# Optimization experiments

Measured on AMD Instinct MI355X. Metric: run time of the kernel, lower is better.

The kernel has to match this reference:

```python
import jax, jax.numpy as jnp
import numpy as np

B, H, I = 131072, 128, 128  # batch, hidden_size, input_size (must be equal per source math)


def setup_inputs() -> dict:
    key = jax.random.key(0)
    ks = jax.random.split(key, 7)
    return {
        "x":   jax.random.normal(ks[0], (B, H), dtype=jnp.float32),
        "h_0": jax.random.normal(ks[1], (B, H), dtype=jnp.float32),
        "c_0": jax.random.normal(ks[2], (B, H), dtype=jnp.float32),
        "ih":  jax.random.normal(ks[3], (4 * H, I), dtype=jnp.float32) * 0.1,
        "hh":  jax.random.normal(ks[4], (4 * H, H), dtype=jnp.float32) * 0.1,
        "ib":  jax.random.normal(ks[5], (4 * H,), dtype=jnp.float32) * 0.1,
        "hb":  jax.random.normal(ks[6], (4 * H,), dtype=jnp.float32) * 0.1,
    }


def reference(x, h_0, c_0, ih, hh, ib, hb):
    hidden = hh.shape[1]
    # torch.split(ih, H) -> 4 chunks [H, I]; gate = x @ chunk (note: NOT chunk.T)
    ih4 = ih.reshape(4, hidden, -1)        # [4, H, I]
    hh4 = hh.reshape(4, hidden, hidden)    # [4, H, H]
    ib4 = ib.reshape(4, 1, hidden)
    hb4 = hb.reshape(4, 1, hidden)
    # combined gate GEMM: gates[g] = x @ ih4[g] + ib4[g] + h_0 @ hh4[g] + hb4[g]
    gates = (jnp.einsum('bh,ghi->gbi', x, ih4)
             + jnp.einsum('bh,ghk->gbk', h_0, hh4)
             + ib4 + hb4)                  # [4, B, H]
    I_g, F_g, G_g, O_g = gates[0], gates[1], gates[2], gates[3]
    c_1 = c_0 * jax.nn.sigmoid(F_g) + jax.nn.sigmoid(I_g) * jnp.tanh(G_g)
    h_1 = jax.nn.sigmoid(O_g) + jnp.tanh(c_1)  # faithful to source (additive, not gated)
    return (h_1, c_1, I_g, F_g, G_g, O_g)
```

## Files before the change

### kernel.cpp

```cpp
#include <hip/hip_runtime.h>
#include <hip/hip_bf16.h>

typedef __attribute__((ext_vector_type(8))) short short8;
typedef __attribute__((ext_vector_type(4))) float f32x4;

#define HSZ 128
#define BM  64
#define NT  512

__device__ __forceinline__ unsigned short f2bf(float f) {
    union { float f; unsigned int u; } c; c.f = f;
    return (unsigned short)((c.u + 0x7FFFu + ((c.u >> 16) & 1u)) >> 16);
}

__global__ void prep_kernel(const float* __restrict__ ih, const float* __restrict__ hh,
                            const float* __restrict__ ib, const float* __restrict__ hb,
                            unsigned short* __restrict__ Wp, float* __restrict__ bias) {
    int tid = blockIdx.x * blockDim.x + threadIdx.x;
    int col = tid >> 5;
    int kg  = tid & 31;
    int g = col >> 7, i = col & 127;
    short8 pk;
    #pragma unroll
    for (int j = 0; j < 8; ++j) {
        int k = kg * 8 + j;
        float v = (k < HSZ) ? ih[(g * HSZ + k) * HSZ + i]
                            : hh[(g * HSZ + (k - HSZ)) * HSZ + i];
        pk[j] = (short)f2bf(v);
    }
    *reinterpret_cast<short8*>(Wp + col * 256 + kg * 8) = pk;
    if (kg == 0) bias[col] = ib[col] + hb[col];
}

union SMem {
    unsigned short A[BM * 264];
    f32x4 O[BM * 32];
};

__global__ __launch_bounds__(NT, 2)
void lstm_kernel(const float* __restrict__ x, const float* __restrict__ h0,
                 const float* __restrict__ c0,
                 const unsigned short* __restrict__ Wp,
                 const float* __restrict__ biasp,
                 float* __restrict__ out, long BH) {
    constexpr int PITCH = 264;
    __shared__ SMem sm;

    const int t = threadIdx.x;
    const long rowBase = (long)blockIdx.x * BM;

    {
        const float4* x4 = reinterpret_cast<const float4*>(x + rowBase * HSZ);
        const float4* h4 = reinterpret_cast<const float4*>(h0 + rowBase * HSZ);
        #pragma unroll
        for (int j = 0; j < 4; ++j) {
            int fi = t + j * NT;
            int row = fi >> 5;
            int c4  = fi & 31;
            float4 vx = x4[fi];
            float4 vh = h4[fi];
            ushort4 px; px.x = f2bf(vx.x); px.y = f2bf(vx.y); px.z = f2bf(vx.z); px.w = f2bf(vx.w);
            ushort4 ph; ph.x = f2bf(vh.x); ph.y = f2bf(vh.y); ph.z = f2bf(vh.z); ph.w = f2bf(vh.w);
            *reinterpret_cast<ushort4*>(&sm.A[row * PITCH + c4 * 4]) = px;
            *reinterpret_cast<ushort4*>(&sm.A[row * PITCH + HSZ + c4 * 4]) = ph;
        }
    }
    __syncthreads();

    const int lane = t & 63;
    const int wid  = t >> 6;
    const int wm = wid & 1;
    const int wn = wid >> 1;
    const int lr = lane & 15;
    const int lk = lane >> 4;

    f32x4 c0v[2][2];
    #pragma unroll
    for (int mi = 0; mi < 2; ++mi)
        #pragma unroll
        for (int ni = 0; ni < 2; ++ni) {
            long pos = (rowBase + wm * 32 + mi * 16 + lr) * HSZ
                     + wn * 32 + ni * 16 + lk * 4;
            c0v[mi][ni] = *reinterpret_cast<const f32x4*>(c0 + pos);
        }

    const char* Ab = reinterpret_cast<const char*>(sm.A)
                   + (wm * 32 + lr) * (PITCH * 2) + lk * 16;
    const char* Wb = reinterpret_cast<const char*>(Wp)
                   + (wn * 32 + lr) * 512 + lk * 16;

    f32x4 acc[2][2][4] = {};

    #pragma unroll
    for (int ks = 0; ks < 8; ++ks) {
        short8 a0 = *reinterpret_cast<const short8*>(Ab + ks * 64);
        short8 a1 = *reinterpret_cast<const short8*>(Ab + 16 * (PITCH * 2) + ks * 64);
        #pragma unroll
        for (int g = 0; g < 4; ++g) {
            #pragma unroll
            for (int ni = 0; ni < 2; ++ni) {
                short8 w = *reinterpret_cast<const short8*>(
                    Wb + (g * 128 + ni * 16) * 512 + ks * 64);
                acc[0][ni][g] = __builtin_amdgcn_mfma_f32_16x16x32_bf16(w, a0, acc[0][ni][g], 0, 0, 0);
                acc[1][ni][g] = __builtin_amdgcn_mfma_f32_16x16x32_bf16(w, a1, acc[1][ni][g], 0, 0, 0);
            }
        }
    }

    #pragma unroll
    for (int ni = 0; ni < 2; ++ni)
        #pragma unroll
        for (int g = 0; g < 4; ++g) {
            f32x4 bg = *reinterpret_cast<const f32x4*>(
                biasp + g * HSZ + wn * 32 + ni * 16 + lk * 4);
            acc[0][ni][g] += bg;
            acc[1][ni][g] += bg;
        }

    __syncthreads();

    int sidx[2][2];
    #pragma unroll
    for (int mi = 0; mi < 2; ++mi)
        #pragma unroll
        for (int ni = 0; ni < 2; ++ni) {
            int row = wm * 32 + mi * 16 + lr;
            sidx[mi][ni] = row * 32 + ((wn * 8 + ni * 4 + lk) ^ (row & 7));
        }

    const long base = rowBase * HSZ;
    auto flush = [&](long obase) {
        #pragma unroll
        for (int p = 0; p < 4; ++p) {
            int f = t + p * NT;
            int row = f >> 5, c = f & 31;
            f32x4 v = sm.O[row * 32 + (c ^ (row & 7))];
            __builtin_nontemporal_store(v,
                reinterpret_cast<f32x4*>(out + obase + (long)f * 4));
        }
    };

    #pragma unroll
    for (int mi = 0; mi < 2; ++mi)
        #pragma unroll
        for (int ni = 0; ni < 2; ++ni) {
            f32x4 v;
            #pragma unroll
            for (int r = 0; r < 4; ++r) {
                float iv = acc[mi][ni][0][r];
                float fv = acc[mi][ni][1][r];
                float gv = acc[mi][ni][2][r];
                float si = 1.f / (1.f + __expf(-iv));
                float sf = 1.f / (1.f + __expf(-fv));
                float tg = 1.f - 2.f / (__expf(2.f * gv) + 1.f);
                v[r] = c0v[mi][ni][r] * sf + si * tg;
            }
            sm.O[sidx[mi][ni]] = v;
        }
    __syncthreads();
    flush(BH + base);
    __syncthreads();

    #pragma unroll
    for (int mi = 0; mi < 2; ++mi)
        #pragma unroll
        for (int ni = 0; ni < 2; ++ni) {
            f32x4 c1 = sm.O[sidx[mi][ni]];
            f32x4 v;
            #pragma unroll
            for (int r = 0; r < 4; ++r) {
                float ov = acc[mi][ni][3][r];
                float so = 1.f / (1.f + __expf(-ov));
                float th = 1.f - 2.f / (__expf(2.f * c1[r]) + 1.f);
                v[r] = so + th;
            }
            sm.O[sidx[mi][ni]] = v;
        }
    __syncthreads();
    flush(base);
    __syncthreads();

    #pragma unroll
    for (int g = 0; g < 4; ++g) {
        #pragma unroll
        for (int mi = 0; mi < 2; ++mi)
            #pragma unroll
            for (int ni = 0; ni < 2; ++ni)
                sm.O[sidx[mi][ni]] = acc[mi][ni][g];
        __syncthreads();
        flush((long)(2 + g) * BH + base);
        if (g < 3) __syncthreads();
    }
}

extern "C" void kernel_launch(void* const* d_in, const int* in_sizes, int n_in,
                              void* d_out, int out_size, void* d_ws, size_t ws_size,
                              hipStream_t stream) {
    const float* x  = (const float*)d_in[0];
    const float* h0 = (const float*)d_in[1];
    const float* c0 = (const float*)d_in[2];
    const float* ih = (const float*)d_in[3];
    const float* hh = (const float*)d_in[4];
    const float* ib = (const float*)d_in[5];
    const float* hb = (const float*)d_in[6];
    float* out = (float*)d_out;

    unsigned short* Wp = (unsigned short*)d_ws;
    float* bias = (float*)((char*)d_ws + 512 * 256 * 2);

    long BH = in_sizes[2];
    long B  = BH / HSZ;

    prep_kernel<<<64, 256, 0, stream>>>(ih, hh, ib, hb, Wp, bias);
    lstm_kernel<<<(int)(B / BM), NT, 0, stream>>>(x, h0, c0, Wp, bias, out, BH);
}
```

Measured before the change: 230.4 us.

## Double-buffer LDS output staging and raise occupancy target in LSTM kernel

The epilogue now uses two LDS staging buffers, so each flush of one tile overlaps with writing the next tile into the other buffer, halving the number of block barriers. The c0 load is moved after the MFMA loop to shorten register live ranges, and launch bounds request 4 blocks per CU instead of 2. LDS per block grows to 64KB, which may itself cap residency, and the tighter register budget could cause spills.

```diff
diff --git a/kernel.cpp b/kernel.cpp
--- a/kernel.cpp
+++ b/kernel.cpp
@@ -34,10 +34,10 @@
 
 union SMem {
     unsigned short A[BM * 264];
-    f32x4 O[BM * 32];
+    f32x4 T[2][BM * 32];
 };
 
-__global__ __launch_bounds__(NT, 2)
+__global__ __launch_bounds__(NT, 4)
 void lstm_kernel(const float* __restrict__ x, const float* __restrict__ h0,
                  const float* __restrict__ c0,
                  const unsigned short* __restrict__ Wp,
@@ -74,16 +74,6 @@
     const int lr = lane & 15;
     const int lk = lane >> 4;
 
-    f32x4 c0v[2][2];
-    #pragma unroll
-    for (int mi = 0; mi < 2; ++mi)
-        #pragma unroll
-        for (int ni = 0; ni < 2; ++ni) {
-            long pos = (rowBase + wm * 32 + mi * 16 + lr) * HSZ
-                     + wn * 32 + ni * 16 + lk * 4;
-            c0v[mi][ni] = *reinterpret_cast<const f32x4*>(c0 + pos);
-        }
-
     const char* Ab = reinterpret_cast<const char*>(sm.A)
                    + (wm * 32 + lr) * (PITCH * 2) + lk * 16;
     const char* Wb = reinterpret_cast<const char*>(Wp)
@@ -107,6 +97,16 @@
         }
     }
 
+    f32x4 c0v[2][2];
+    #pragma unroll
+    for (int mi = 0; mi < 2; ++mi)
+        #pragma unroll
+        for (int ni = 0; ni < 2; ++ni) {
+            long pos = (rowBase + wm * 32 + mi * 16 + lr) * HSZ
+                     + wn * 32 + ni * 16 + lk * 4;
+            c0v[mi][ni] = *reinterpret_cast<const f32x4*>(c0 + pos);
+        }
+
     #pragma unroll
     for (int ni = 0; ni < 2; ++ni)
         #pragma unroll
@@ -119,22 +119,16 @@
 
     __syncthreads();
 
-    int sidx[2][2];
-    #pragma unroll
-    for (int mi = 0; mi < 2; ++mi)
-        #pragma unroll
-        for (int ni = 0; ni < 2; ++ni) {
-            int row = wm * 32 + mi * 16 + lr;
-            sidx[mi][ni] = row * 32 + ((wn * 8 + ni * 4 + lk) ^ (row & 7));
-        }
-
     const long base = rowBase * HSZ;
-    auto flush = [&](long obase) {
+    #define SIDX(mi, ni) ((wm*32 + (mi)*16 + lr) * 32 + \
+                          ((wn*8 + (ni)*4 + lk) ^ ((wm*32 + (mi)*16 + lr) & 7)))
+
+    auto flush = [&](const f32x4* T, long obase) {
         #pragma unroll
         for (int p = 0; p < 4; ++p) {
             int f = t + p * NT;
             int row = f >> 5, c = f & 31;
-            f32x4 v = sm.O[row * 32 + (c ^ (row & 7))];
+            f32x4 v = T[row * 32 + (c ^ (row & 7))];
             __builtin_nontemporal_store(v,
                 reinterpret_cast<f32x4*>(out + obase + (long)f * 4));
         }
@@ -155,17 +149,16 @@
                 float tg = 1.f - 2.f / (__expf(2.f * gv) + 1.f);
                 v[r] = c0v[mi][ni][r] * sf + si * tg;
             }
-            sm.O[sidx[mi][ni]] = v;
-        }
-    __syncthreads();
-    flush(BH + base);
-    __syncthreads();
-
+            sm.T[0][SIDX(mi, ni)] = v;
+        }
+    __syncthreads();
+
+    flush(sm.T[0], BH + base);
     #pragma unroll
     for (int mi = 0; mi < 2; ++mi)
         #pragma unroll
         for (int ni = 0; ni < 2; ++ni) {
-            f32x4 c1 = sm.O[sidx[mi][ni]];
+            f32x4 c1 = sm.T[0][SIDX(mi, ni)];
             f32x4 v;
             #pragma unroll
             for (int r = 0; r < 4; ++r) {
@@ -174,23 +167,44 @@
                 float th = 1.f - 2.f / (__expf(2.f * c1[r]) + 1.f);
                 v[r] = so + th;
             }
-            sm.O[sidx[mi][ni]] = v;
-        }
-    __syncthreads();
-    flush(base);
-    __syncthreads();
-
-    #pragma unroll
-    for (int g = 0; g < 4; ++g) {
-        #pragma unroll
-        for (int mi = 0; mi < 2; ++mi)
-            #pragma unroll
-            for (int ni = 0; ni < 2; ++ni)
-                sm.O[sidx[mi][ni]] = acc[mi][ni][g];
-        __syncthreads();
-        flush((long)(2 + g) * BH + base);
-        if (g < 3) __syncthreads();
-    }
+            sm.T[1][SIDX(mi, ni)] = v;
+        }
+    __syncthreads();
+
+    flush(sm.T[1], base);
+    #pragma unroll
+    for (int mi = 0; mi < 2; ++mi)
+        #pragma unroll
+        for (int ni = 0; ni < 2; ++ni)
+            sm.T[0][SIDX(mi, ni)] = acc[mi][ni][0];
+    __syncthreads();
+
+    flush(sm.T[0], 2 * BH + base);
+    #pragma unroll
+    for (int mi = 0; mi < 2; ++mi)
+        #pragma unroll
+        for (int ni = 0; ni < 2; ++ni)
+            sm.T[1][SIDX(mi, ni)] = acc[mi][ni][1];
+    __syncthreads();
+
+    flush(sm.T[1], 3 * BH + base);
+    #pragma unroll
+    for (int mi = 0; mi < 2; ++mi)
+        #pragma unroll
+        for (int ni = 0; ni < 2; ++ni)
+            sm.T[0][SIDX(mi, ni)] = acc[mi][ni][2];
+    __syncthreads();
+
+    flush(sm.T[0], 4 * BH + base);
+    #pragma unroll
+    for (int mi = 0; mi < 2; ++mi)
+        #pragma unroll
+        for (int ni = 0; ni < 2; ++ni)
+            sm.T[1][SIDX(mi, ni)] = acc[mi][ni][3];
+    __syncthreads();
+
+    flush(sm.T[1], 5 * BH + base);
+    #undef SIDX
 }
 
 extern "C" void kernel_launch(void* const* d_in, const int* in_sizes, int n_in,
```

Measured after the change: 206.0 us. 10.6% less time.

## Use per-wave LDS staging for output transposes instead of block-wide barriers

Applied to the files above, without the earlier changes.

The epilogue now stages each wave's own 32x32 output tiles in a private LDS region and synchronises with wave barriers only, so the six block-wide __syncthreads around each output flush go away. c1 and h1 are computed in a single pass instead of being round-tripped through shared memory. The c0 load moves after the MFMA loop and launch bounds rise to 4 blocks per CU, trading register headroom for occupancy. Each wave now writes 32-row by 128-byte segments instead of full contiguous block rows, which may reduce store coalescing.

```diff
diff --git a/kernel.cpp b/kernel.cpp
--- a/kernel.cpp
+++ b/kernel.cpp
@@ -34,10 +34,10 @@
 
 union SMem {
     unsigned short A[BM * 264];
-    f32x4 O[BM * 32];
+    float T[8][2048];
 };
 
-__global__ __launch_bounds__(NT, 2)
+__global__ __launch_bounds__(NT, 4)
 void lstm_kernel(const float* __restrict__ x, const float* __restrict__ h0,
                  const float* __restrict__ c0,
                  const unsigned short* __restrict__ Wp,
@@ -74,16 +74,6 @@
     const int lr = lane & 15;
     const int lk = lane >> 4;
 
-    f32x4 c0v[2][2];
-    #pragma unroll
-    for (int mi = 0; mi < 2; ++mi)
-        #pragma unroll
-        for (int ni = 0; ni < 2; ++ni) {
-            long pos = (rowBase + wm * 32 + mi * 16 + lr) * HSZ
-                     + wn * 32 + ni * 16 + lk * 4;
-            c0v[mi][ni] = *reinterpret_cast<const f32x4*>(c0 + pos);
-        }
-
     const char* Ab = reinterpret_cast<const char*>(sm.A)
                    + (wm * 32 + lr) * (PITCH * 2) + lk * 16;
     const char* Wb = reinterpret_cast<const char*>(Wp)
@@ -107,6 +97,16 @@
         }
     }
 
+    f32x4 c0v[2][2];
+    #pragma unroll
+    for (int mi = 0; mi < 2; ++mi)
+        #pragma unroll
+        for (int ni = 0; ni < 2; ++ni) {
+            long pos = (rowBase + wm * 32 + mi * 16 + lr) * HSZ
+                     + wn * 32 + ni * 16 + lk * 4;
+            c0v[mi][ni] = *reinterpret_cast<const f32x4*>(c0 + pos);
+        }
+
     #pragma unroll
     for (int ni = 0; ni < 2; ++ni)
         #pragma unroll
@@ -119,77 +119,74 @@
 
     __syncthreads();
 
-    int sidx[2][2];
+    float* wt = sm.T[wid];
+    const long rbase = (rowBase + wm * 32) * (long)HSZ + wn * 32;
+    const int rr0 = lane >> 3;
+    const int gg0 = lane & 7;
+
     #pragma unroll
     for (int mi = 0; mi < 2; ++mi)
         #pragma unroll
         for (int ni = 0; ni < 2; ++ni) {
-            int row = wm * 32 + mi * 16 + lr;
-            sidx[mi][ni] = row * 32 + ((wn * 8 + ni * 4 + lk) ^ (row & 7));
-        }
-
-    const long base = rowBase * HSZ;
-    auto flush = [&](long obase) {
-        #pragma unroll
-        for (int p = 0; p < 4; ++p) {
-            int f = t + p * NT;
-            int row = f >> 5, c = f & 31;
-            f32x4 v = sm.O[row * 32 + (c ^ (row & 7))];
-            __builtin_nontemporal_store(v,
-                reinterpret_cast<f32x4*>(out + obase + (long)f * 4));
-        }
-    };
-
-    #pragma unroll
-    for (int mi = 0; mi < 2; ++mi)
-        #pragma unroll
-        for (int ni = 0; ni < 2; ++ni) {
-            f32x4 v;
+            int row = mi * 16 + lr;
+            int g4  = ni * 4 + lk;
+            f32x4 c1v, h1v;
             #pragma unroll
             for (int r = 0; r < 4; ++r) {
                 float iv = acc[mi][ni][0][r];
                 float fv = acc[mi][ni][1][r];
                 float gv = acc[mi][ni][2][r];
+                float ov = acc[mi][ni][3][r];
                 float si = 1.f / (1.f + __expf(-iv));
                 float sf = 1.f / (1.f + __expf(-fv));
                 float tg = 1.f - 2.f / (__expf(2.f * gv) + 1.f);
-                v[r] = c0v[mi][ni][r] * sf + si * tg;
+                float so = 1.f / (1.f + __expf(-ov));
+                float c1 = c0v[mi][ni][r] * sf + si * tg;
+                float th = 1.f - 2.f / (__expf(2.f * c1) + 1.f);
+                c1v[r] = c1;
+                h1v[r] = so + th;
             }
-            sm.O[sidx[mi][ni]] = v;
-        }
-    __syncthreads();
-    flush(BH + base);
-    __syncthreads();
-
-    #pragma unroll
-    for (int mi = 0; mi < 2; ++mi)
-        #pragma unroll
-        for (int ni = 0; ni < 2; ++ni) {
-            f32x4 c1 = sm.O[sidx[mi][ni]];
-            f32x4 v;
-            #pragma unroll
-            for (int r = 0; r < 4; ++r) {
-                float ov = acc[mi][ni][3][r];
-                float so = 1.f / (1.f + __expf(-ov));
-                float th = 1.f - 2.f / (__expf(2.f * c1[r]) + 1.f);
-                v[r] = so + th;
-            }
-            sm.O[sidx[mi][ni]] = v;
-        }
-    __syncthreads();
-    flush(base);
-    __syncthreads();
+            int idx = row * 32 + ((g4 ^ (row & 7)) * 4);
+            *reinterpret_cast<f32x4*>(&wt[idx])        = c1v;
+            *reinterpret_cast<f32x4*>(&wt[1024 + idx]) = h1v;
+        }
+    __builtin_amdgcn_wave_barrier();
+
+    #pragma unroll
+    for (int p = 0; p < 4; ++p) {
+        int rr  = p * 8 + rr0;
+        int idx = rr * 32 + ((gg0 ^ (rr & 7)) * 4);
+        f32x4 vc = *reinterpret_cast<const f32x4*>(&wt[idx]);
+        f32x4 vh = *reinterpret_cast<const f32x4*>(&wt[1024 + idx]);
+        long rpos = rbase + (long)rr * HSZ + gg0 * 4;
+        __builtin_nontemporal_store(vc, reinterpret_cast<f32x4*>(out + BH + rpos));
+        __builtin_nontemporal_store(vh, reinterpret_cast<f32x4*>(out + rpos));
+    }
+    __builtin_amdgcn_wave_barrier();
 
     #pragma unroll
     for (int g = 0; g < 4; ++g) {
+        float* slot = wt + (g & 1) * 1024;
         #pragma unroll
         for (int mi = 0; mi < 2; ++mi)
             #pragma unroll
-            for (int ni = 0; ni < 2; ++ni)
-                sm.O[sidx[mi][ni]] = acc[mi][ni][g];
-        __syncthreads();
-        flush((long)(2 + g) * BH + base);
-        if (g < 3) __syncthreads();
+            for (int ni = 0; ni < 2; ++ni) {
+                int row = mi * 16 + lr;
+                int g4  = ni * 4 + lk;
+                int idx = row * 32 + ((g4 ^ (row & 7)) * 4);
+                *reinterpret_cast<f32x4*>(&slot[idx]) = acc[mi][ni][g];
+            }
+        __builtin_amdgcn_wave_barrier();
+        #pragma unroll
+        for (int p = 0; p < 4; ++p) {
+            int rr  = p * 8 + rr0;
+            int idx = rr * 32 + ((gg0 ^ (rr & 7)) * 4);
+            f32x4 v = *reinterpret_cast<const f32x4*>(&slot[idx]);
+            long rpos = rbase + (long)rr * HSZ + gg0 * 4;
+            __builtin_nontemporal_store(v,
+                reinterpret_cast<f32x4*>(out + (long)(2 + g) * BH + rpos));
+        }
+        __builtin_amdgcn_wave_barrier();
     }
 }
 
```

Result: faster. 209.6 us (-9.0%).
